# Performance work log

Hardware: AMD Instinct MI355X
Metric: run time of the kernel (lower is better)

The kernel has to match this reference:

```python
import jax, jax.numpy as jnp
import numpy as np

N_NODES = 100000
EPS = 1e-12  # F.normalize eps


def _glorot(key, shape):
    fan_in, fan_out = shape[0], shape[1]
    lim = (6.0 / (fan_in + fan_out)) ** 0.5
    return jax.random.uniform(key, shape, jnp.float32, -lim, lim)


def setup_inputs() -> dict:
    key = jax.random.key(0)
    ks = jax.random.split(key, 8)
    d_in, d_hid, d_out = 128, 128, 64
    x = jax.random.normal(ks[0], (N_NODES, d_in), jnp.float32)
    edge_index = jax.random.randint(ks[1], (2, 1600000), 0, N_NODES, jnp.int32)
    return {
        "x": x,
        "edge_index": edge_index,
        "Wl1": _glorot(ks[2], (d_in, d_hid)),
        "Wr1": _glorot(ks[3], (d_in, d_hid)),
        "b1": jnp.zeros((d_hid,), jnp.float32),
        "Wl2": _glorot(ks[4], (d_hid, d_out)),
        "Wr2": _glorot(ks[5], (d_hid, d_out)),
        "b2": jnp.zeros((d_out,), jnp.float32),
    }


def _sage_conv(x, src, dst, Wl, Wr, b):
    # gather source-node features per edge, max-aggregate onto destinations
    msgs = x[src]                                   # [E, d]
    agg = jax.ops.segment_max(msgs, dst, num_segments=N_NODES)
    # PyG scatter-max leaves 0 for nodes with no incoming edges
    agg = jnp.where(jnp.isneginf(agg), 0.0, agg)    # [N, d]
    out = agg @ Wl + x @ Wr + b                     # lin_l(aggr) + lin_r(root)
    # normalize=True -> L2 normalize rows (F.normalize semantics)
    norm = jnp.maximum(jnp.linalg.norm(out, axis=-1, keepdims=True), EPS)
    return out / norm


def reference(x, edge_index, Wl1, Wr1, b1, Wl2, Wr2, b2):
    src, dst = edge_index[0], edge_index[1]
    # dropout p=0.9 is identity in eval mode
    h = jax.nn.relu(_sage_conv(x, src, dst, Wl1, Wr1, b1))
    return _sage_conv(h, src, dst, Wl2, Wr2, b2)
```

## Files before the change

### kernel.cpp

```cpp
#include <hip/hip_runtime.h>
#include <math.h>

typedef __attribute__((ext_vector_type(8))) short short8;
typedef __attribute__((ext_vector_type(4))) float floatx4;

static __device__ __forceinline__ ushort f32_to_bf16_rne(float f) {
  union { float f; unsigned int i; } c;
  c.f = f;
  unsigned int lsb = (c.i >> 16) & 1u;
  c.i += 0x7fffu + lsb;
  return (ushort)(c.i >> 16);
}
static __device__ __forceinline__ float bf16_lo(unsigned int v) {
  union { unsigned int i; float f; } c;
  c.i = v << 16;
  return c.f;
}
static __device__ __forceinline__ float bf16_hi(unsigned int v) {
  union { unsigned int i; float f; } c;
  c.i = v & 0xffff0000u;
  return c.f;
}


#define NBLK 256

__global__ __launch_bounds__(256) void binhist_kernel(const int* __restrict__ dst,
                                                      int* __restrict__ bh, int E, int EBLK,
                                                      int NBUCKET) {
  __shared__ int h[256];
  int t = threadIdx.x, blk = blockIdx.x;
  h[t] = 0;
  __syncthreads();
  int e0 = blk * EBLK, e1 = min(E, e0 + EBLK);
  for (int e = e0 + t; e < e1; e += 256) atomicAdd(&h[__builtin_nontemporal_load(dst + e) >> 9], 1);
  __syncthreads();
  if (t < NBUCKET) bh[t * NBLK + blk] = h[t];
}

__global__ void scan1_kernel(const int* __restrict__ counts, int* __restrict__ offsets,
                             int* __restrict__ tileSums, int N) {
  __shared__ int sd[256];
  int t = threadIdx.x;
  int base = blockIdx.x * 1024 + t * 4;
  int v[4];
#pragma unroll
  for (int i = 0; i < 4; i++) v[i] = (base + i < N) ? counts[base + i] : 0;
  int s = v[0] + v[1] + v[2] + v[3];
  sd[t] = s;
  __syncthreads();
  int acc = s;
  for (int off = 1; off < 256; off <<= 1) {
    int add = (t >= off) ? sd[t - off] : 0;
    __syncthreads();
    acc += add;
    sd[t] = acc;
    __syncthreads();
  }
  int run = acc - s;
#pragma unroll
  for (int i = 0; i < 4; i++) {
    if (base + i < N) offsets[base + i] = run;
    run += v[i];
  }
  if (t == 255) tileSums[blockIdx.x] = acc;
}

__global__ void scan2_kernel(int* __restrict__ tileSums, int nT) {
  __shared__ int sd[128];
  int t = threadIdx.x;
  int v = (t < nT) ? tileSums[t] : 0;
  sd[t] = v;
  __syncthreads();
  int acc = v;
  for (int off = 1; off < 128; off <<= 1) {
    int add = (t >= off) ? sd[t - off] : 0;
    __syncthreads();
    acc += add;
    sd[t] = acc;
    __syncthreads();
  }
  if (t < nT) tileSums[t] = acc - v;
}

__global__ void scan3_nc_kernel(int* __restrict__ offsets, const int* __restrict__ tileSums,
                                int N) {
  int i = blockIdx.x * 256 + threadIdx.x;
  if (i >= N) return;
  offsets[i] += tileSums[i >> 10];
}

__global__ __launch_bounds__(256) void binscatter_kernel(const int* __restrict__ src,
                                                         const int* __restrict__ dst,
                                                         const int* __restrict__ bhOff,
                                                         unsigned int* __restrict__ binned, int E,
                                                         int EBLK, int NBUCKET) {
  __shared__ int cur[256];
  int t = threadIdx.x, blk = blockIdx.x;
  if (t < NBUCKET) cur[t] = bhOff[t * NBLK + blk];
  __syncthreads();
  int e0 = blk * EBLK, e1 = min(E, e0 + EBLK);
  for (int e = e0 + t; e < e1; e += 256) {
    int d = __builtin_nontemporal_load(dst + e);
    int s = __builtin_nontemporal_load(src + e);
    int pos = atomicAdd(&cur[d >> 9], 1);
    binned[pos] = ((unsigned int)(d & 511) << 17) | (unsigned int)s;
  }
}

__global__ __launch_bounds__(256) void bucket_build_kernel(
    const unsigned int* __restrict__ binned, const int* __restrict__ bhOff,
    int* __restrict__ counts, int* __restrict__ offsets, int* __restrict__ csr, int N, int E,
    int NBUCKET) {
  __shared__ int h[512];
  __shared__ int lofs[512];
  __shared__ int cur[512];
  __shared__ int sd[256];
  int b = blockIdx.x, t = threadIdx.x;
  int S = bhOff[b * NBLK];
  int Send = (b + 1 < NBUCKET) ? bhOff[(b + 1) * NBLK] : E;
  h[t] = 0;
  h[t + 256] = 0;
  __syncthreads();
  for (int e = S + t; e < Send; e += 256) {
    unsigned int rv = __builtin_nontemporal_load(binned + e);
    atomicAdd(&h[(rv >> 17) & 511], 1);
  }
  __syncthreads();
  int h0 = h[2 * t], h1 = h[2 * t + 1];
  int s = h0 + h1;
  sd[t] = s;
  __syncthreads();
  int acc = s;
  for (int off = 1; off < 256; off <<= 1) {
    int add = (t >= off) ? sd[t - off] : 0;
    __syncthreads();
    acc += add;
    sd[t] = acc;
    __syncthreads();
  }
  int run = acc - s;
  lofs[2 * t] = run;
  lofs[2 * t + 1] = run + h0;
  __syncthreads();
  int node0 = b * 512;
#pragma unroll
  for (int i = 0; i < 2; i++) {
    int l = t + i * 256;
    int node = node0 + l;
    if (node < N) {
      counts[node] = h[l];
      offsets[node] = S + lofs[l];
    }
    cur[l] = S + lofs[l];
  }
  __syncthreads();
  for (int e = S + t; e < Send; e += 256) {
    unsigned int rv = __builtin_nontemporal_load(binned + e);
    int pos = atomicAdd(&cur[(rv >> 17) & 511], 1);
    csr[pos] = (int)(rv & 0x1ffffu);
  }
}


__global__ void f32_to_bf16_kernel(const float* __restrict__ in, ushort* __restrict__ out, int n) {
  int i = (blockIdx.x * 256 + threadIdx.x) * 8;
  if (i >= n) return;
  float4 a = *(const float4*)(in + i);
  float4 b = *(const float4*)(in + i + 4);
  union { ushort u[8]; short8 v; } r;
  r.u[0] = f32_to_bf16_rne(a.x); r.u[1] = f32_to_bf16_rne(a.y);
  r.u[2] = f32_to_bf16_rne(a.z); r.u[3] = f32_to_bf16_rne(a.w);
  r.u[4] = f32_to_bf16_rne(b.x); r.u[5] = f32_to_bf16_rne(b.y);
  r.u[6] = f32_to_bf16_rne(b.z); r.u[7] = f32_to_bf16_rne(b.w);
  *(short8*)(out + i) = r.v;
}

__global__ void wt_conv_all_kernel(const float* __restrict__ Wl1, const float* __restrict__ Wr1,
                                   const float* __restrict__ Wl2, const float* __restrict__ Wr2,
                                   ushort* __restrict__ WlT1, ushort* __restrict__ WrT1,
                                   ushort* __restrict__ WlT2, ushort* __restrict__ WrT2) {
  int idx = blockIdx.x * 256 + threadIdx.x;
  const float* W;
  ushort* WT;
  int C, base;
  if (idx < 16384)      { W = Wl1; WT = WlT1; C = 128; base = idx; }
  else if (idx < 32768) { W = Wr1; WT = WrT1; C = 128; base = idx - 16384; }
  else if (idx < 40960) { W = Wl2; WT = WlT2; C = 64;  base = idx - 32768; }
  else                  { W = Wr2; WT = WrT2; C = 64;  base = idx - 40960; }
  int k = base / C, c = base % C;
  WT[c * 128 + k] = f32_to_bf16_rne(W[base]);
}


__global__ __launch_bounds__(256) void agg_max_bf16_kernel(
    const ushort* __restrict__ feat, const int* __restrict__ csr,
    const int* __restrict__ offsets, const int* __restrict__ counts,
    unsigned int* __restrict__ aggb, int N) {
  int lane = threadIdx.x & 63;
  int node = __builtin_amdgcn_readfirstlane((int)((blockIdx.x * 256 + threadIdx.x) >> 6));
  if (node >= N) return;
  const unsigned int* fu = (const unsigned int*)feat;
  int start = offsets[node];
  int deg = counts[node];
  float m0 = 0.0f, m1 = 0.0f;
  if (deg > 0) {
    m0 = -INFINITY;
    m1 = -INFINITY;
    const int* ce = csr + start;
    int e = 0;
    for (; e + 8 <= deg; e += 8) {
      int s0 = ce[e + 0], s1 = ce[e + 1], s2 = ce[e + 2], s3 = ce[e + 3];
      int s4 = ce[e + 4], s5 = ce[e + 5], s6 = ce[e + 6], s7 = ce[e + 7];
      unsigned int v0 = fu[(size_t)s0 * 64 + lane];
      unsigned int v1 = fu[(size_t)s1 * 64 + lane];
      unsigned int v2 = fu[(size_t)s2 * 64 + lane];
      unsigned int v3 = fu[(size_t)s3 * 64 + lane];
      unsigned int v4 = fu[(size_t)s4 * 64 + lane];
      unsigned int v5 = fu[(size_t)s5 * 64 + lane];
      unsigned int v6 = fu[(size_t)s6 * 64 + lane];
      unsigned int v7 = fu[(size_t)s7 * 64 + lane];
      m0 = fmaxf(m0, fmaxf(fmaxf(bf16_lo(v0), bf16_lo(v1)), fmaxf(bf16_lo(v2), bf16_lo(v3))));
      m0 = fmaxf(m0, fmaxf(fmaxf(bf16_lo(v4), bf16_lo(v5)), fmaxf(bf16_lo(v6), bf16_lo(v7))));
      m1 = fmaxf(m1, fmaxf(fmaxf(bf16_hi(v0), bf16_hi(v1)), fmaxf(bf16_hi(v2), bf16_hi(v3))));
      m1 = fmaxf(m1, fmaxf(fmaxf(bf16_hi(v4), bf16_hi(v5)), fmaxf(bf16_hi(v6), bf16_hi(v7))));
    }
    for (; e < deg; e++) {
      unsigned int v = fu[(size_t)ce[e] * 64 + lane];
      m0 = fmaxf(m0, bf16_lo(v));
      m1 = fmaxf(m1, bf16_hi(v));
    }
  }
  unsigned int res = (__float_as_uint(m0) >> 16) | (__float_as_uint(m1) & 0xffff0000u);
  aggb[(size_t)node * 64 + lane] = res;
}


template <int DOUT, bool RELU, bool OUTBF16>
__global__ __launch_bounds__(256) void gemm_mfma_kernel(
    const ushort* __restrict__ A, const ushort* __restrict__ X, const ushort* __restrict__ WlT,
    const ushort* __restrict__ WrT, const float* __restrict__ bias, void* __restrict__ outp,
    int N) {
  constexpr int D = 128;
  constexpr int NCT = DOUT / 16;
  int t = threadIdx.x;
  int lane = t & 63;
  int wid = t >> 6;
  int l16 = lane & 15;
  int lk = lane >> 4;
  int rowbase = blockIdx.x * 128 + wid * 32;

  floatx4 acc[2][NCT];
#pragma unroll
  for (int rt = 0; rt < 2; rt++)
#pragma unroll
    for (int ct = 0; ct < NCT; ct++) acc[rt][ct] = (floatx4){0.f, 0.f, 0.f, 0.f};

  int ra = rowbase + l16;       if (ra > N - 1) ra = N - 1;
  int rb = rowbase + 16 + l16;  if (rb > N - 1) rb = N - 1;
  const ushort* pA0 = A + (size_t)ra * D;
  const ushort* pA1 = A + (size_t)rb * D;
  const ushort* pX0 = X + (size_t)ra * D;
  const ushort* pX1 = X + (size_t)rb * D;

#pragma unroll
  for (int kc = 0; kc < 4; kc++) {
    int ko = kc * 32 + lk * 8;
    short8 a0 = *(const short8*)(pA0 + ko);
    short8 a1 = *(const short8*)(pA1 + ko);
    short8 x0 = *(const short8*)(pX0 + ko);
    short8 x1 = *(const short8*)(pX1 + ko);
#pragma unroll
    for (int ct = 0; ct < NCT; ct++) {
      int c = ct * 16 + l16;
      short8 bl = *(const short8*)(WlT + (size_t)c * D + ko);
      short8 br = *(const short8*)(WrT + (size_t)c * D + ko);
      acc[0][ct] = __builtin_amdgcn_mfma_f32_16x16x32_bf16(a0, bl, acc[0][ct], 0, 0, 0);
      acc[0][ct] = __builtin_amdgcn_mfma_f32_16x16x32_bf16(x0, br, acc[0][ct], 0, 0, 0);
      acc[1][ct] = __builtin_amdgcn_mfma_f32_16x16x32_bf16(a1, bl, acc[1][ct], 0, 0, 0);
      acc[1][ct] = __builtin_amdgcn_mfma_f32_16x16x32_bf16(x1, br, acc[1][ct], 0, 0, 0);
    }
  }

  float bb[NCT];
#pragma unroll
  for (int ct = 0; ct < NCT; ct++) bb[ct] = bias[ct * 16 + l16];
#pragma unroll
  for (int rt = 0; rt < 2; rt++)
#pragma unroll
    for (int ct = 0; ct < NCT; ct++)
#pragma unroll
      for (int r = 0; r < 4; r++) acc[rt][ct][r] += bb[ct];

#pragma unroll
  for (int rt = 0; rt < 2; rt++) {
#pragma unroll
    for (int r = 0; r < 4; r++) {
      float ss = 0.f;
#pragma unroll
      for (int ct = 0; ct < NCT; ct++) ss += acc[rt][ct][r] * acc[rt][ct][r];
      ss += __shfl_xor(ss, 1);
      ss += __shfl_xor(ss, 2);
      ss += __shfl_xor(ss, 4);
      ss += __shfl_xor(ss, 8);
      float inv = 1.0f / fmaxf(sqrtf(ss), 1e-12f);
      int n = rowbase + rt * 16 + lk * 4 + r;
      if (n < N) {
#pragma unroll
        for (int ct = 0; ct < NCT; ct++) {
          float v = acc[rt][ct][r] * inv;
          if (RELU) v = fmaxf(v, 0.f);
          size_t o = (size_t)n * DOUT + ct * 16 + l16;
          if (OUTBF16)
            ((ushort*)outp)[o] = f32_to_bf16_rne(v);
          else
            ((float*)outp)[o] = v;
        }
      }
    }
  }
}


extern "C" void kernel_launch(void* const* d_in, const int* in_sizes, int n_in, void* d_out,
                              int out_size, void* d_ws, size_t ws_size, hipStream_t stream) {
  const float* x = (const float*)d_in[0];
  const int* ei = (const int*)d_in[1];
  const float* Wl1 = (const float*)d_in[2];
  const float* Wr1 = (const float*)d_in[3];
  const float* b1 = (const float*)d_in[4];
  const float* Wl2 = (const float*)d_in[5];
  const float* Wr2 = (const float*)d_in[6];
  const float* b2 = (const float*)d_in[7];
  float* out = (float*)d_out;

  const int E = in_sizes[1] / 2;
  const int N = in_sizes[0] / 128;
  const int D = 128;

  const int* src = ei;
  const int* dst = ei + E;

  char* w = (char*)d_ws;
  size_t off = 0;
  auto alloc = [&](size_t bytes) {
    void* p = w + off;
    off = (off + bytes + 511) & ~((size_t)511);
    return p;
  };
  const int NBUCKET = (N + 511) >> 9;
  const int M = NBUCKET * NBLK;
  int* bh = (int*)alloc((size_t)M * 4);
  int* tileSums = (int*)alloc(512);
  int* counts = (int*)alloc((size_t)N * 4);
  int* offsets = (int*)alloc((size_t)N * 4);
  unsigned int* binned = (unsigned int*)alloc((size_t)E * 4);
  int* csr = (int*)alloc((size_t)E * 4);
  ushort* xb = (ushort*)alloc((size_t)N * D * 2);
  ushort* aggb = (ushort*)alloc((size_t)N * D * 2);
  ushort* hb = (ushort*)alloc((size_t)N * D * 2);
  ushort* WlT1 = (ushort*)alloc(128 * 128 * 2);
  ushort* WrT1 = (ushort*)alloc(128 * 128 * 2);
  ushort* WlT2 = (ushort*)alloc(128 * 64 * 2);
  ushort* WrT2 = (ushort*)alloc(128 * 64 * 2);
  (void)ws_size;

  const int EBLK = (E + NBLK - 1) / NBLK;
  const int nTiles = (M + 1023) / 1024;

  binhist_kernel<<<NBLK, 256, 0, stream>>>(dst, bh, E, EBLK, NBUCKET);
  scan1_kernel<<<nTiles, 256, 0, stream>>>(bh, bh, tileSums, M);
  scan2_kernel<<<1, 128, 0, stream>>>(tileSums, nTiles);
  scan3_nc_kernel<<<(M + 255) / 256, 256, 0, stream>>>(bh, tileSums, M);
  binscatter_kernel<<<NBLK, 256, 0, stream>>>(src, dst, bh, binned, E, EBLK, NBUCKET);
  bucket_build_kernel<<<NBUCKET, 256, 0, stream>>>(binned, bh, counts, offsets, csr, N, E,
                                                   NBUCKET);

  f32_to_bf16_kernel<<<(N * D / 8 + 255) / 256, 256, 0, stream>>>(x, xb, N * D);
  wt_conv_all_kernel<<<192, 256, 0, stream>>>(Wl1, Wr1, Wl2, Wr2, WlT1, WrT1, WlT2, WrT2);

  const int nbGemm = (N + 127) / 128;

  agg_max_bf16_kernel<<<(N * 64 + 255) / 256, 256, 0, stream>>>(xb, csr, offsets, counts,
                                                                (unsigned int*)aggb, N);
  gemm_mfma_kernel<128, true, true>
      <<<nbGemm, 256, 0, stream>>>(aggb, xb, WlT1, WrT1, b1, hb, N);

  agg_max_bf16_kernel<<<(N * 64 + 255) / 256, 256, 0, stream>>>(hb, csr, offsets, counts,
                                                                (unsigned int*)aggb, N);
  gemm_mfma_kernel<64, false, false>
      <<<nbGemm, 256, 0, stream>>>(aggb, hb, WlT2, WrT2, b2, out, N);
}
```

Measured before the change: 361.5 us.

## Fuse CSR histogram and scatter into per-block local sort with fewer launches

Replaces the histogram, three-pass global scan and global scatter with a single kernel that loads each block's edges into registers, sorts them by bucket in shared memory, and writes contiguous per-block runs. A small single-block scan then computes bucket starts, and the bucket build kernel gathers its segments from each block's run using a binary search over per-block lengths. Offsets and counts are packed into one int2 array so the aggregation kernel does a single load per node. This cuts kernel launches and one full pass over the edge list, at the cost of a per-element binary search, a fixed MAXPER register bound that assumes at most 26 edges per thread, and a 25KB shared sort buffer.

```diff
diff --git a/kernel.cpp b/kernel.cpp
--- a/kernel.cpp
+++ b/kernel.cpp
@@ -24,32 +24,79 @@
 
 
 #define NBLK 256
-
-__global__ __launch_bounds__(256) void binhist_kernel(const int* __restrict__ dst,
-                                                      int* __restrict__ bh, int E, int EBLK,
-                                                      int NBUCKET) {
+#define MAXPER 26
+
+__global__ __launch_bounds__(256) void binsort_kernel(const int* __restrict__ src,
+                                                      const int* __restrict__ dst,
+                                                      int* __restrict__ bh2,
+                                                      unsigned int* __restrict__ binned2, int E,
+                                                      int EBLK, int NBUCKET) {
   __shared__ int h[256];
+  __shared__ int lstart[256];
+  __shared__ int cursor[256];
+  __shared__ int sd[256];
+  __shared__ unsigned int sorted[6272];
   int t = threadIdx.x, blk = blockIdx.x;
+  int e0 = blk * EBLK, e1 = min(E, e0 + EBLK);
+  int ds[MAXPER], ss[MAXPER];
+  int cnt = 0;
   h[t] = 0;
   __syncthreads();
-  int e0 = blk * EBLK, e1 = min(E, e0 + EBLK);
-  for (int e = e0 + t; e < e1; e += 256) atomicAdd(&h[__builtin_nontemporal_load(dst + e) >> 9], 1);
-  __syncthreads();
-  if (t < NBUCKET) bh[t * NBLK + blk] = h[t];
-}
-
-__global__ void scan1_kernel(const int* __restrict__ counts, int* __restrict__ offsets,
-                             int* __restrict__ tileSums, int N) {
+#pragma unroll
+  for (int i = 0; i < MAXPER; i++) {
+    int e = e0 + t + i * 256;
+    if (e < e1) {
+      ds[i] = __builtin_nontemporal_load(dst + e);
+      ss[i] = __builtin_nontemporal_load(src + e);
+      atomicAdd(&h[ds[i] >> 9], 1);
+      cnt = i + 1;
+    }
+  }
+  __syncthreads();
+  int v = h[t];
+  sd[t] = v;
+  __syncthreads();
+  int acc = v;
+  for (int off = 1; off < 256; off <<= 1) {
+    int add = (t >= off) ? sd[t - off] : 0;
+    __syncthreads();
+    acc += add;
+    sd[t] = acc;
+    __syncthreads();
+  }
+  int start = acc - v;
+  lstart[t] = start;
+  cursor[t] = start;
+  if (t < NBUCKET) bh2[t * NBLK + blk] = start;
+  if (t == 0) bh2[NBUCKET * NBLK + blk] = e1 - e0;
+  __syncthreads();
+#pragma unroll
+  for (int i = 0; i < MAXPER; i++) {
+    if (i < cnt) {
+      int d = ds[i];
+      int pos = atomicAdd(&cursor[d >> 9], 1);
+      sorted[pos] = ((unsigned int)(d & 511) << 17) | (unsigned int)ss[i];
+    }
+  }
+  __syncthreads();
+  int n = e1 - e0;
+  for (int i = t; i < n; i += 256) binned2[(size_t)e0 + i] = sorted[i];
+}
+
+__global__ void bucketscan_kernel(const int* __restrict__ bh2, int* __restrict__ bucketStart,
+                                  int NBUCKET) {
   __shared__ int sd[256];
   int t = threadIdx.x;
-  int base = blockIdx.x * 1024 + t * 4;
-  int v[4];
-#pragma unroll
-  for (int i = 0; i < 4; i++) v[i] = (base + i < N) ? counts[base + i] : 0;
-  int s = v[0] + v[1] + v[2] + v[3];
-  sd[t] = s;
-  __syncthreads();
-  int acc = s;
+  int tot = 0;
+  if (t < NBUCKET) {
+    const int* r0 = bh2 + (size_t)t * NBLK;
+    const int* r1 = bh2 + (size_t)(t + 1) * NBLK;
+#pragma unroll 8
+    for (int i = 0; i < NBLK; i++) tot += r1[i] - r0[i];
+  }
+  sd[t] = tot;
+  __syncthreads();
+  int acc = tot;
   for (int off = 1; off < 256; off <<= 1) {
     int add = (t >= off) ? sd[t - off] : 0;
     __syncthreads();
@@ -57,106 +104,84 @@
     sd[t] = acc;
     __syncthreads();
   }
-  int run = acc - s;
-#pragma unroll
-  for (int i = 0; i < 4; i++) {
-    if (base + i < N) offsets[base + i] = run;
-    run += v[i];
-  }
-  if (t == 255) tileSums[blockIdx.x] = acc;
-}
-
-__global__ void scan2_kernel(int* __restrict__ tileSums, int nT) {
-  __shared__ int sd[128];
-  int t = threadIdx.x;
-  int v = (t < nT) ? tileSums[t] : 0;
-  sd[t] = v;
-  __syncthreads();
-  int acc = v;
-  for (int off = 1; off < 128; off <<= 1) {
-    int add = (t >= off) ? sd[t - off] : 0;
-    __syncthreads();
-    acc += add;
-    sd[t] = acc;
-    __syncthreads();
-  }
-  if (t < nT) tileSums[t] = acc - v;
-}
-
-__global__ void scan3_nc_kernel(int* __restrict__ offsets, const int* __restrict__ tileSums,
-                                int N) {
-  int i = blockIdx.x * 256 + threadIdx.x;
-  if (i >= N) return;
-  offsets[i] += tileSums[i >> 10];
-}
-
-__global__ __launch_bounds__(256) void binscatter_kernel(const int* __restrict__ src,
-                                                         const int* __restrict__ dst,
-                                                         const int* __restrict__ bhOff,
-                                                         unsigned int* __restrict__ binned, int E,
-                                                         int EBLK, int NBUCKET) {
-  __shared__ int cur[256];
-  int t = threadIdx.x, blk = blockIdx.x;
-  if (t < NBUCKET) cur[t] = bhOff[t * NBLK + blk];
-  __syncthreads();
-  int e0 = blk * EBLK, e1 = min(E, e0 + EBLK);
-  for (int e = e0 + t; e < e1; e += 256) {
-    int d = __builtin_nontemporal_load(dst + e);
-    int s = __builtin_nontemporal_load(src + e);
-    int pos = atomicAdd(&cur[d >> 9], 1);
-    binned[pos] = ((unsigned int)(d & 511) << 17) | (unsigned int)s;
-  }
-}
-
-__global__ __launch_bounds__(256) void bucket_build_kernel(
-    const unsigned int* __restrict__ binned, const int* __restrict__ bhOff,
-    int* __restrict__ counts, int* __restrict__ offsets, int* __restrict__ csr, int N, int E,
-    int NBUCKET) {
+  if (t < NBUCKET) bucketStart[t] = acc - tot;
+}
+
+__global__ __launch_bounds__(256) void bucket_build2_kernel(
+    const unsigned int* __restrict__ binned2, const int* __restrict__ bh2,
+    const int* __restrict__ bucketStart, int2* __restrict__ offcnt, int* __restrict__ csr, int N,
+    int EBLK, int NBUCKET) {
+  __shared__ int ls0[256];
+  __shared__ int dof[257];
   __shared__ int h[512];
-  __shared__ int lofs[512];
   __shared__ int cur[512];
   __shared__ int sd[256];
   int b = blockIdx.x, t = threadIdx.x;
-  int S = bhOff[b * NBLK];
-  int Send = (b + 1 < NBUCKET) ? bhOff[(b + 1) * NBLK] : E;
+  int l0 = bh2[(size_t)b * NBLK + t];
+  int l1 = bh2[(size_t)(b + 1) * NBLK + t];
+  int len = l1 - l0;
+  ls0[t] = l0;
+  sd[t] = len;
+  __syncthreads();
+  int acc = len;
+  for (int off = 1; off < 256; off <<= 1) {
+    int add = (t >= off) ? sd[t - off] : 0;
+    __syncthreads();
+    acc += add;
+    sd[t] = acc;
+    __syncthreads();
+  }
+  dof[t] = acc - len;
+  if (t == 255) dof[256] = acc;
   h[t] = 0;
   h[t + 256] = 0;
   __syncthreads();
-  for (int e = S + t; e < Send; e += 256) {
-    unsigned int rv = __builtin_nontemporal_load(binned + e);
+  int tot = dof[256];
+  int S = bucketStart[b];
+  for (int i = t; i < tot; i += 256) {
+    int lo = 0, hi = 255;
+    while (lo < hi) {
+      int mid = (lo + hi + 1) >> 1;
+      if (dof[mid] <= i) lo = mid; else hi = mid - 1;
+    }
+    unsigned int rv = binned2[(size_t)lo * EBLK + ls0[lo] + (i - dof[lo])];
     atomicAdd(&h[(rv >> 17) & 511], 1);
   }
   __syncthreads();
   int h0 = h[2 * t], h1 = h[2 * t + 1];
-  int s = h0 + h1;
-  sd[t] = s;
-  __syncthreads();
-  int acc = s;
+  int s2 = h0 + h1;
+  sd[t] = s2;
+  __syncthreads();
+  int a2 = s2;
   for (int off = 1; off < 256; off <<= 1) {
     int add = (t >= off) ? sd[t - off] : 0;
     __syncthreads();
-    acc += add;
-    sd[t] = acc;
-    __syncthreads();
-  }
-  int run = acc - s;
-  lofs[2 * t] = run;
-  lofs[2 * t + 1] = run + h0;
-  __syncthreads();
+    a2 += add;
+    sd[t] = a2;
+    __syncthreads();
+  }
+  int run = a2 - s2;
   int node0 = b * 512;
-#pragma unroll
-  for (int i = 0; i < 2; i++) {
-    int l = t + i * 256;
+  {
+    int l = 2 * t;
     int node = node0 + l;
-    if (node < N) {
-      counts[node] = h[l];
-      offsets[node] = S + lofs[l];
-    }
-    cur[l] = S + lofs[l];
-  }
-  __syncthreads();
-  for (int e = S + t; e < Send; e += 256) {
-    unsigned int rv = __builtin_nontemporal_load(binned + e);
+    int st = S + run;
+    if (node < N) offcnt[node] = make_int2(st, h0);
+    cur[l] = st;
+    l = 2 * t + 1;
+    node = node0 + l;
+    st = S + run + h0;
+    if (node < N) offcnt[node] = make_int2(st, h1);
+    cur[l] = st;
+  }
+  __syncthreads();
+  for (int i = t; i < tot; i += 256) {
+    int lo = 0, hi = 255;
+    while (lo < hi) {
+      int mid = (lo + hi + 1) >> 1;
+      if (dof[mid] <= i) lo = mid; else hi = mid - 1;
+    }
+    unsigned int rv = binned2[(size_t)lo * EBLK + ls0[lo] + (i - dof[lo])];
     int pos = atomicAdd(&cur[(rv >> 17) & 511], 1);
     csr[pos] = (int)(rv & 0x1ffffu);
   }
@@ -195,14 +220,14 @@
 
 __global__ __launch_bounds__(256) void agg_max_bf16_kernel(
     const ushort* __restrict__ feat, const int* __restrict__ csr,
-    const int* __restrict__ offsets, const int* __restrict__ counts,
-    unsigned int* __restrict__ aggb, int N) {
+    const int2* __restrict__ offcnt, unsigned int* __restrict__ aggb, int N) {
   int lane = threadIdx.x & 63;
   int node = __builtin_amdgcn_readfirstlane((int)((blockIdx.x * 256 + threadIdx.x) >> 6));
   if (node >= N) return;
   const unsigned int* fu = (const unsigned int*)feat;
-  int start = offsets[node];
-  int deg = counts[node];
+  int2 oc = offcnt[node];
+  int start = oc.x;
+  int deg = oc.y;
   float m0 = 0.0f, m1 = 0.0f;
   if (deg > 0) {
     m0 = -INFINITY;
@@ -349,12 +374,10 @@
     return p;
   };
   const int NBUCKET = (N + 511) >> 9;
-  const int M = NBUCKET * NBLK;
-  int* bh = (int*)alloc((size_t)M * 4);
-  int* tileSums = (int*)alloc(512);
-  int* counts = (int*)alloc((size_t)N * 4);
-  int* offsets = (int*)alloc((size_t)N * 4);
-  unsigned int* binned = (unsigned int*)alloc((size_t)E * 4);
+  int* bh2 = (int*)alloc((size_t)(NBUCKET + 1) * NBLK * 4);
+  int* bucketStart = (int*)alloc((size_t)NBUCKET * 4);
+  int2* offcnt = (int2*)alloc((size_t)N * 8);
+  unsigned int* binned2 = (unsigned int*)alloc((size_t)E * 4);
   int* csr = (int*)alloc((size_t)E * 4);
   ushort* xb = (ushort*)alloc((size_t)N * D * 2);
   ushort* aggb = (ushort*)alloc((size_t)N * D * 2);
@@ -366,27 +389,23 @@
   (void)ws_size;
 
   const int EBLK = (E + NBLK - 1) / NBLK;
-  const int nTiles = (M + 1023) / 1024;
-
-  binhist_kernel<<<NBLK, 256, 0, stream>>>(dst, bh, E, EBLK, NBUCKET);
-  scan1_kernel<<<nTiles, 256, 0, stream>>>(bh, bh, tileSums, M);
-  scan2_kernel<<<1, 128, 0, stream>>>(tileSums, nTiles);
-  scan3_nc_kernel<<<(M + 255) / 256, 256, 0, stream>>>(bh, tileSums, M);
-  binscatter_kernel<<<NBLK, 256, 0, stream>>>(src, dst, bh, binned, E, EBLK, NBUCKET);
-  bucket_build_kernel<<<NBUCKET, 256, 0, stream>>>(binned, bh, counts, offsets, csr, N, E,
-                                                   NBUCKET);
+
+  binsort_kernel<<<NBLK, 256, 0, stream>>>(src, dst, bh2, binned2, E, EBLK, NBUCKET);
+  bucketscan_kernel<<<1, 256, 0, stream>>>(bh2, bucketStart, NBUCKET);
+  bucket_build2_kernel<<<NBUCKET, 256, 0, stream>>>(binned2, bh2, bucketStart, offcnt, csr, N,
+                                                    EBLK, NBUCKET);
 
   f32_to_bf16_kernel<<<(N * D / 8 + 255) / 256, 256, 0, stream>>>(x, xb, N * D);
   wt_conv_all_kernel<<<192, 256, 0, stream>>>(Wl1, Wr1, Wl2, Wr2, WlT1, WrT1, WlT2, WrT2);
 
   const int nbGemm = (N + 127) / 128;
 
-  agg_max_bf16_kernel<<<(N * 64 + 255) / 256, 256, 0, stream>>>(xb, csr, offsets, counts,
+  agg_max_bf16_kernel<<<(N * 64 + 255) / 256, 256, 0, stream>>>(xb, csr, offcnt,
                                                                 (unsigned int*)aggb, N);
   gemm_mfma_kernel<128, true, true>
       <<<nbGemm, 256, 0, stream>>>(aggb, xb, WlT1, WrT1, b1, hb, N);
 
-  agg_max_bf16_kernel<<<(N * 64 + 255) / 256, 256, 0, stream>>>(hb, csr, offsets, counts,
+  agg_max_bf16_kernel<<<(N * 64 + 255) / 256, 256, 0, stream>>>(hb, csr, offcnt,
                                                                 (unsigned int*)aggb, N);
   gemm_mfma_kernel<64, false, false>
       <<<nbGemm, 256, 0, stream>>>(aggb, hb, WlT2, WrT2, b2, out, N);
```

Measured after the change: 383.5 us. 1.06x slower.

## Fuse max aggregation into MFMA GEMM via swizzled LDS tile

Applied to the files above, without the earlier changes.

Merges the per-node max-aggregation kernel with the following bf16 MFMA GEMM: each block aggregates 64 nodes into a swizzled LDS tile, then runs the GEMM and L2-normalize on it. This removes the global write and re-read of the aggregated buffer and two kernel launches. Offsets and counts are packed into one int2 so each node needs a single load. In exchange, each wave now aggregates 16 nodes serially with less parallelism per node, which may hurt load balance and latency hiding in the gather phase.

```diff
diff --git a/kernel.cpp b/kernel.cpp
--- a/kernel.cpp
+++ b/kernel.cpp
@@ -110,8 +110,7 @@
 
 __global__ __launch_bounds__(256) void bucket_build_kernel(
     const unsigned int* __restrict__ binned, const int* __restrict__ bhOff,
-    int* __restrict__ counts, int* __restrict__ offsets, int* __restrict__ csr, int N, int E,
-    int NBUCKET) {
+    int2* __restrict__ offcnt, int* __restrict__ csr, int N, int E, int NBUCKET) {
   __shared__ int h[512];
   __shared__ int lofs[512];
   __shared__ int cur[512];
@@ -148,11 +147,9 @@
   for (int i = 0; i < 2; i++) {
     int l = t + i * 256;
     int node = node0 + l;
-    if (node < N) {
-      counts[node] = h[l];
-      offsets[node] = S + lofs[l];
-    }
-    cur[l] = S + lofs[l];
+    int st = S + lofs[l];
+    if (node < N) offcnt[node] = make_int2(st, h[l]);
+    cur[l] = st;
   }
   __syncthreads();
   for (int e = S + t; e < Send; e += 256) {
@@ -193,92 +190,89 @@
 }
 
 
-__global__ __launch_bounds__(256) void agg_max_bf16_kernel(
+#define SWZ(r, j) ((r) * 64 + ((((j) >> 2) ^ ((r) & 15)) << 2) + ((j) & 3))
+
+template <int DOUT, bool RELU, bool OUTBF16>
+__global__ __launch_bounds__(256, 5) void fused_agg_gemm_kernel(
     const ushort* __restrict__ feat, const int* __restrict__ csr,
-    const int* __restrict__ offsets, const int* __restrict__ counts,
-    unsigned int* __restrict__ aggb, int N) {
-  int lane = threadIdx.x & 63;
-  int node = __builtin_amdgcn_readfirstlane((int)((blockIdx.x * 256 + threadIdx.x) >> 6));
-  if (node >= N) return;
-  const unsigned int* fu = (const unsigned int*)feat;
-  int start = offsets[node];
-  int deg = counts[node];
-  float m0 = 0.0f, m1 = 0.0f;
-  if (deg > 0) {
-    m0 = -INFINITY;
-    m1 = -INFINITY;
-    const int* ce = csr + start;
-    int e = 0;
-    for (; e + 8 <= deg; e += 8) {
-      int s0 = ce[e + 0], s1 = ce[e + 1], s2 = ce[e + 2], s3 = ce[e + 3];
-      int s4 = ce[e + 4], s5 = ce[e + 5], s6 = ce[e + 6], s7 = ce[e + 7];
-      unsigned int v0 = fu[(size_t)s0 * 64 + lane];
-      unsigned int v1 = fu[(size_t)s1 * 64 + lane];
-      unsigned int v2 = fu[(size_t)s2 * 64 + lane];
-      unsigned int v3 = fu[(size_t)s3 * 64 + lane];
-      unsigned int v4 = fu[(size_t)s4 * 64 + lane];
-      unsigned int v5 = fu[(size_t)s5 * 64 + lane];
-      unsigned int v6 = fu[(size_t)s6 * 64 + lane];
-      unsigned int v7 = fu[(size_t)s7 * 64 + lane];
-      m0 = fmaxf(m0, fmaxf(fmaxf(bf16_lo(v0), bf16_lo(v1)), fmaxf(bf16_lo(v2), bf16_lo(v3))));
-      m0 = fmaxf(m0, fmaxf(fmaxf(bf16_lo(v4), bf16_lo(v5)), fmaxf(bf16_lo(v6), bf16_lo(v7))));
-      m1 = fmaxf(m1, fmaxf(fmaxf(bf16_hi(v0), bf16_hi(v1)), fmaxf(bf16_hi(v2), bf16_hi(v3))));
-      m1 = fmaxf(m1, fmaxf(fmaxf(bf16_hi(v4), bf16_hi(v5)), fmaxf(bf16_hi(v6), bf16_hi(v7))));
-    }
-    for (; e < deg; e++) {
-      unsigned int v = fu[(size_t)ce[e] * 64 + lane];
-      m0 = fmaxf(m0, bf16_lo(v));
-      m1 = fmaxf(m1, bf16_hi(v));
-    }
-  }
-  unsigned int res = (__float_as_uint(m0) >> 16) | (__float_as_uint(m1) & 0xffff0000u);
-  aggb[(size_t)node * 64 + lane] = res;
-}
-
-
-template <int DOUT, bool RELU, bool OUTBF16>
-__global__ __launch_bounds__(256) void gemm_mfma_kernel(
-    const ushort* __restrict__ A, const ushort* __restrict__ X, const ushort* __restrict__ WlT,
+    const int2* __restrict__ offcnt, const ushort* __restrict__ WlT,
     const ushort* __restrict__ WrT, const float* __restrict__ bias, void* __restrict__ outp,
     int N) {
   constexpr int D = 128;
   constexpr int NCT = DOUT / 16;
+  __shared__ unsigned int sA[4096];
+
   int t = threadIdx.x;
   int lane = t & 63;
-  int wid = t >> 6;
+  int widr = t >> 6;
+  int node0 = blockIdx.x * 64;
+  const unsigned int* fu = (const unsigned int*)feat;
+
+  for (int i = 0; i < 16; i++) {
+    int node = __builtin_amdgcn_readfirstlane(node0 + widr * 16 + i);
+    int r = widr * 16 + i;
+    float m0 = 0.0f, m1 = 0.0f;
+    if (node < N) {
+      int2 oc = offcnt[node];
+      int deg = oc.y;
+      if (deg > 0) {
+        m0 = -INFINITY;
+        m1 = -INFINITY;
+        const int* ce = csr + oc.x;
+        int e = 0;
+        for (; e + 8 <= deg; e += 8) {
+          int s0 = ce[e + 0], s1 = ce[e + 1], s2 = ce[e + 2], s3 = ce[e + 3];
+          int s4 = ce[e + 4], s5 = ce[e + 5], s6 = ce[e + 6], s7 = ce[e + 7];
+          unsigned int v0 = fu[(size_t)s0 * 64 + lane];
+          unsigned int v1 = fu[(size_t)s1 * 64 + lane];
+          unsigned int v2 = fu[(size_t)s2 * 64 + lane];
+          unsigned int v3 = fu[(size_t)s3 * 64 + lane];
+          unsigned int v4 = fu[(size_t)s4 * 64 + lane];
+          unsigned int v5 = fu[(size_t)s5 * 64 + lane];
+          unsigned int v6 = fu[(size_t)s6 * 64 + lane];
+          unsigned int v7 = fu[(size_t)s7 * 64 + lane];
+          m0 = fmaxf(m0, fmaxf(fmaxf(bf16_lo(v0), bf16_lo(v1)), fmaxf(bf16_lo(v2), bf16_lo(v3))));
+          m0 = fmaxf(m0, fmaxf(fmaxf(bf16_lo(v4), bf16_lo(v5)), fmaxf(bf16_lo(v6), bf16_lo(v7))));
+          m1 = fmaxf(m1, fmaxf(fmaxf(bf16_hi(v0), bf16_hi(v1)), fmaxf(bf16_hi(v2), bf16_hi(v3))));
+          m1 = fmaxf(m1, fmaxf(fmaxf(bf16_hi(v4), bf16_hi(v5)), fmaxf(bf16_hi(v6), bf16_hi(v7))));
+        }
+        for (; e < deg; e++) {
+          unsigned int v = fu[(size_t)ce[e] * 64 + lane];
+          m0 = fmaxf(m0, bf16_lo(v));
+          m1 = fmaxf(m1, bf16_hi(v));
+        }
+      }
+    }
+    unsigned int res = (__float_as_uint(m0) >> 16) | (__float_as_uint(m1) & 0xffff0000u);
+    sA[SWZ(r, lane)] = res;
+  }
+  __syncthreads();
+
   int l16 = lane & 15;
   int lk = lane >> 4;
-  int rowbase = blockIdx.x * 128 + wid * 32;
-
-  floatx4 acc[2][NCT];
-#pragma unroll
-  for (int rt = 0; rt < 2; rt++)
-#pragma unroll
-    for (int ct = 0; ct < NCT; ct++) acc[rt][ct] = (floatx4){0.f, 0.f, 0.f, 0.f};
-
-  int ra = rowbase + l16;       if (ra > N - 1) ra = N - 1;
-  int rb = rowbase + 16 + l16;  if (rb > N - 1) rb = N - 1;
-  const ushort* pA0 = A + (size_t)ra * D;
-  const ushort* pA1 = A + (size_t)rb * D;
-  const ushort* pX0 = X + (size_t)ra * D;
-  const ushort* pX1 = X + (size_t)rb * D;
+  int rowbase = node0 + widr * 16;
+  int rloc = widr * 16 + l16;
+
+  floatx4 acc[NCT];
+#pragma unroll
+  for (int ct = 0; ct < NCT; ct++) acc[ct] = (floatx4){0.f, 0.f, 0.f, 0.f};
+
+  int ra = rowbase + l16;
+  if (ra > N - 1) ra = N - 1;
+  const ushort* pX0 = feat + (size_t)ra * D;
 
 #pragma unroll
   for (int kc = 0; kc < 4; kc++) {
     int ko = kc * 32 + lk * 8;
-    short8 a0 = *(const short8*)(pA0 + ko);
-    short8 a1 = *(const short8*)(pA1 + ko);
+    short8 a0 = *(const short8*)((const ushort*)(sA + rloc * 64 + (((kc * 4 + lk) ^ l16) << 2)));
     short8 x0 = *(const short8*)(pX0 + ko);
-    short8 x1 = *(const short8*)(pX1 + ko);
 #pragma unroll
     for (int ct = 0; ct < NCT; ct++) {
       int c = ct * 16 + l16;
       short8 bl = *(const short8*)(WlT + (size_t)c * D + ko);
       short8 br = *(const short8*)(WrT + (size_t)c * D + ko);
-      acc[0][ct] = __builtin_amdgcn_mfma_f32_16x16x32_bf16(a0, bl, acc[0][ct], 0, 0, 0);
-      acc[0][ct] = __builtin_amdgcn_mfma_f32_16x16x32_bf16(x0, br, acc[0][ct], 0, 0, 0);
-      acc[1][ct] = __builtin_amdgcn_mfma_f32_16x16x32_bf16(a1, bl, acc[1][ct], 0, 0, 0);
-      acc[1][ct] = __builtin_amdgcn_mfma_f32_16x16x32_bf16(x1, br, acc[1][ct], 0, 0, 0);
+      acc[ct] = __builtin_amdgcn_mfma_f32_16x16x32_bf16(a0, bl, acc[ct], 0, 0, 0);
+      acc[ct] = __builtin_amdgcn_mfma_f32_16x16x32_bf16(x0, br, acc[ct], 0, 0, 0);
     }
   }
 
@@ -286,36 +280,31 @@
 #pragma unroll
   for (int ct = 0; ct < NCT; ct++) bb[ct] = bias[ct * 16 + l16];
 #pragma unroll
-  for (int rt = 0; rt < 2; rt++)
-#pragma unroll
-    for (int ct = 0; ct < NCT; ct++)
-#pragma unroll
-      for (int r = 0; r < 4; r++) acc[rt][ct][r] += bb[ct];
-
-#pragma unroll
-  for (int rt = 0; rt < 2; rt++) {
-#pragma unroll
-    for (int r = 0; r < 4; r++) {
-      float ss = 0.f;
-#pragma unroll
-      for (int ct = 0; ct < NCT; ct++) ss += acc[rt][ct][r] * acc[rt][ct][r];
-      ss += __shfl_xor(ss, 1);
-      ss += __shfl_xor(ss, 2);
-      ss += __shfl_xor(ss, 4);
-      ss += __shfl_xor(ss, 8);
-      float inv = 1.0f / fmaxf(sqrtf(ss), 1e-12f);
-      int n = rowbase + rt * 16 + lk * 4 + r;
-      if (n < N) {
-#pragma unroll
-        for (int ct = 0; ct < NCT; ct++) {
-          float v = acc[rt][ct][r] * inv;
-          if (RELU) v = fmaxf(v, 0.f);
-          size_t o = (size_t)n * DOUT + ct * 16 + l16;
-          if (OUTBF16)
-            ((ushort*)outp)[o] = f32_to_bf16_rne(v);
-          else
-            ((float*)outp)[o] = v;
-        }
+  for (int ct = 0; ct < NCT; ct++)
+#pragma unroll
+    for (int r = 0; r < 4; r++) acc[ct][r] += bb[ct];
+
+#pragma unroll
+  for (int r = 0; r < 4; r++) {
+    float ss = 0.f;
+#pragma unroll
+    for (int ct = 0; ct < NCT; ct++) ss += acc[ct][r] * acc[ct][r];
+    ss += __shfl_xor(ss, 1);
+    ss += __shfl_xor(ss, 2);
+    ss += __shfl_xor(ss, 4);
+    ss += __shfl_xor(ss, 8);
+    float inv = 1.0f / fmaxf(sqrtf(ss), 1e-12f);
+    int n = rowbase + lk * 4 + r;
+    if (n < N) {
+#pragma unroll
+      for (int ct = 0; ct < NCT; ct++) {
+        float v = acc[ct][r] * inv;
+        if (RELU) v = fmaxf(v, 0.f);
+        size_t o = (size_t)n * DOUT + ct * 16 + l16;
+        if (OUTBF16)
+          ((ushort*)outp)[o] = f32_to_bf16_rne(v);
+        else
+          ((float*)outp)[o] = v;
       }
     }
   }
@@ -352,12 +341,10 @@
   const int M = NBUCKET * NBLK;
   int* bh = (int*)alloc((size_t)M * 4);
   int* tileSums = (int*)alloc(512);
-  int* counts = (int*)alloc((size_t)N * 4);
-  int* offsets = (int*)alloc((size_t)N * 4);
+  int2* offcnt = (int2*)alloc((size_t)N * 8);
   unsigned int* binned = (unsigned int*)alloc((size_t)E * 4);
   int* csr = (int*)alloc((size_t)E * 4);
   ushort* xb = (ushort*)alloc((size_t)N * D * 2);
-  ushort* aggb = (ushort*)alloc((size_t)N * D * 2);
   ushort* hb = (ushort*)alloc((size_t)N * D * 2);
   ushort* WlT1 = (ushort*)alloc(128 * 128 * 2);
   ushort* WrT1 = (ushort*)alloc(128 * 128 * 2);
@@ -373,21 +360,16 @@
   scan2_kernel<<<1, 128, 0, stream>>>(tileSums, nTiles);
   scan3_nc_kernel<<<(M + 255) / 256, 256, 0, stream>>>(bh, tileSums, M);
   binscatter_kernel<<<NBLK, 256, 0, stream>>>(src, dst, bh, binned, E, EBLK, NBUCKET);
-  bucket_build_kernel<<<NBUCKET, 256, 0, stream>>>(binned, bh, counts, offsets, csr, N, E,
-                                                   NBUCKET);
+  bucket_build_kernel<<<NBUCKET, 256, 0, stream>>>(binned, bh, offcnt, csr, N, E, NBUCKET);
 
   f32_to_bf16_kernel<<<(N * D / 8 + 255) / 256, 256, 0, stream>>>(x, xb, N * D);
   wt_conv_all_kernel<<<192, 256, 0, stream>>>(Wl1, Wr1, Wl2, Wr2, WlT1, WrT1, WlT2, WrT2);
 
-  const int nbGemm = (N + 127) / 128;
-
-  agg_max_bf16_kernel<<<(N * 64 + 255) / 256, 256, 0, stream>>>(xb, csr, offsets, counts,
-                                                                (unsigned int*)aggb, N);
-  gemm_mfma_kernel<128, true, true>
-      <<<nbGemm, 256, 0, stream>>>(aggb, xb, WlT1, WrT1, b1, hb, N);
-
-  agg_max_bf16_kernel<<<(N * 64 + 255) / 256, 256, 0, stream>>>(hb, csr, offsets, counts,
-                                                                (unsigned int*)aggb, N);
-  gemm_mfma_kernel<64, false, false>
-      <<<nbGemm, 256, 0, stream>>>(aggb, hb, WlT2, WrT2, b2, out, N);
-}
+  const int nbFused = (N + 63) / 64;
+
+  fused_agg_gemm_kernel<128, true, true>
+      <<<nbFused, 256, 0, stream>>>(xb, csr, offcnt, WlT1, WrT1, b1, hb, N);
+
+  fused_agg_gemm_kernel<64, false, false>
+      <<<nbFused, 256, 0, stream>>>(hb, csr, offcnt, WlT2, WrT2, b2, out, N);
+}
```

Result: slower. 388.8 us (+7.6%).
